# Optimization experiments

Measured on AMD Instinct MI355X. Metric: run time of the kernel, lower is better.

Reference implementation:

```python
import jax, jax.numpy as jnp
import numpy as np

B, T, F, H = 8192, 96, 64, 256


def setup_inputs() -> dict:
    key = jax.random.key(0)
    ks = jax.random.split(key, 8)
    s = 0.05
    return {
        "decoder_feature": jax.random.normal(ks[0], (B, T, F), jnp.float32),
        "init_state": jax.random.normal(ks[1], (B, H), jnp.float32),
        "decoder_init_input": jax.random.normal(ks[2], (B, 1), jnp.float32),
        "kernel": jax.random.normal(ks[3], (1 + F, 3 * H), jnp.float32) * s,
        "recurrent_kernel": jax.random.normal(ks[4], (H, 3 * H), jnp.float32) * s,
        "input_bias": jnp.zeros((3 * H,), jnp.float32),
        "recurrent_bias": jnp.zeros((3 * H,), jnp.float32),
        "dense_w": jax.random.normal(ks[5], (H, 1), jnp.float32) * s,
        "dense_b": jnp.zeros((1,), jnp.float32),
        "predict_seq_length": T,
    }


def reference(decoder_feature, init_state, decoder_init_input, kernel,
              recurrent_kernel, input_bias, recurrent_bias, dense_w, dense_b,
              predict_seq_length):
    # teacher=None, use_attention=False path of Decoder2.forward.
    # Keras GRUCell (reset_after=True) recurrence, scanned over time.
    feats = jnp.swapaxes(decoder_feature[:, :predict_seq_length, :], 0, 1)  # [T,B,F]

    def step(carry, feat_t):
        prev_out, h = carry                                   # [B,1], [B,H]
        x = jnp.concatenate([prev_out, feat_t], axis=-1)      # [B,1+F]
        mx = x @ kernel + input_bias                          # [B,3H]
        mh = h @ recurrent_kernel + recurrent_bias            # [B,3H]
        xz, xr, xh = jnp.split(mx, 3, axis=-1)
        hz, hr, hh = jnp.split(mh, 3, axis=-1)
        z = jax.nn.sigmoid(xz + hz)
        r = jax.nn.sigmoid(xr + hr)
        cand = jnp.tanh(xh + r * hh)
        h_new = z * h + (1.0 - z) * cand
        out = h_new @ dense_w + dense_b                       # [B,1]
        return (out, h_new), out

    _, outs = jax.lax.scan(step, (decoder_init_input, init_state), feats)
    return jnp.swapaxes(outs, 0, 1)                           # [B,T,1]
```

## Files before the change

kernel.cpp:

```cpp
#include <hip/hip_runtime.h>


#define Bdim 8192
#define Tdim 96
#define Fdim 64
#define Hdim 256
#define BM   32
#define XS   72
#define HS   264
#define OS   97

typedef __attribute__((ext_vector_type(8))) short s16x8;
typedef __attribute__((ext_vector_type(4))) float f32x4;

#define MFMA __builtin_amdgcn_mfma_f32_16x16x32_bf16

__device__ __forceinline__ unsigned short f2bf(float f) {
    union { float f; unsigned u; } v; v.f = f;
    unsigned r = v.u + 0x7FFFu + ((v.u >> 16) & 1u);
    return (unsigned short)(r >> 16);
}

__device__ __forceinline__ float sigm_fast(float x) {
    return __builtin_amdgcn_rcpf(1.0f + __expf(-x));
}
__device__ __forceinline__ float tanh_fast(float x) {
    return 1.0f - 2.0f * __builtin_amdgcn_rcpf(1.0f + __expf(2.0f * x));
}

__global__ void prep_swz(const float* __restrict__ Wk, const float* __restrict__ Wr,
                         unsigned short* __restrict__ sW) {
    int idx = blockIdx.x * blockDim.x + threadIdx.x;
    if (idx >= 480 * 64) return;
    int lane = idx & 63, f = idx >> 6;
    int n2 = f & 1;
    int g  = (f >> 1) % 3;
    int kt = (f / 6) % 10;
    int w  = f / 60;
    int q = lane >> 4, cc = lane & 15;
    int n = g * 256 + w * 32 + n2 * 16 + cc;
    unsigned short* d = sW + (size_t)idx * 8;
#pragma unroll
    for (int j = 0; j < 8; ++j) {
        float v;
        if (kt < 8) v = Wr[(size_t)(kt * 32 + q * 8 + j) * 768 + n];
        else        v = Wk[(size_t)(1 + (kt - 8) * 32 + q * 8 + j) * 768 + n];
        d[j] = f2bf(v);
    }
}

__launch_bounds__(1024)
__global__ void gru_mfma9(
    const float* __restrict__ feat,
    const float* __restrict__ init_state,
    const float* __restrict__ init_inp,
    const unsigned short* __restrict__ sW,
    const float* __restrict__ Wk,
    const float* __restrict__ ib, const float* __restrict__ rb,
    const float* __restrict__ dw, const float* __restrict__ db,
    float* __restrict__ out)
{
    __shared__ __align__(16) unsigned short xs[2][BM * XS];
    __shared__ __align__(16) unsigned short hs[2][BM * HS];
    __shared__ float wpart[2][16][BM];
    __shared__ float outbuf[BM * OS];

    const int tid  = threadIdx.x;
    const int lane = tid & 63;
    const int wv   = tid >> 6;
    const int q    = lane >> 4;
    const int c    = lane & 15;
    const int b0   = blockIdx.x * BM;
    const int col  = wv * 16 + c;

    const float bz   = ib[col]       + rb[col];
    const float brr  = ib[256 + col] + rb[256 + col];
    const float bxh  = ib[512 + col];
    const float bhh  = rb[512 + col];
    const float wk0z = Wk[col];
    const float wk0r = Wk[256 + col];
    const float wk0h = Wk[512 + col];
    const float dwv  = dw[col];
    const float dbv  = db[0];

    float hreg[2][4];
    float prevreg[2][4];
#pragma unroll
    for (int mt = 0; mt < 2; ++mt)
#pragma unroll
        for (int i = 0; i < 4; ++i) {
            int row = mt * 16 + q * 4 + i;
            prevreg[mt][i] = init_inp[b0 + row];
            float v = init_state[(size_t)(b0 + row) * Hdim + col];
            hreg[mt][i] = v;
            hs[0][row * HS + col] = f2bf(v);
        }

    {
        int r = tid >> 5, fi = tid & 31;
        float2 f = *(const float2*)&feat[((size_t)(b0 + r) * Tdim + 0) * Fdim + fi * 2];
        ushort2 p; p.x = f2bf(f.x); p.y = f2bf(f.y);
        *(ushort2*)&xs[0][r * XS + fi * 2] = p;
    }

    const unsigned short* wp0 =
        sW + ((size_t)(wv >> 1) * 60 + (wv & 1)) * 512 + lane * 8;

    s16x8 bf[2][3];
#pragma unroll
    for (int g = 0; g < 3; ++g)
        bf[0][g] = *(const s16x8*)(wp0 + (size_t)g * 1024);

    __syncthreads();

    for (int t = 0; t < Tdim; ++t) {
        const unsigned short* hsp = hs[t & 1];
        const unsigned short* xsp = xs[t & 1];

        f32x4 az[2], ar[2], ax[2], ah[2];
#pragma unroll
        for (int mt = 0; mt < 2; ++mt) {
            az[mt] = (f32x4)0.0f; ar[mt] = (f32x4)0.0f;
            ax[mt] = (f32x4)0.0f; ah[mt] = (f32x4)0.0f;
        }

#pragma unroll
        for (int kt = 0; kt < 10; ++kt) {
            if (kt + 1 < 10) {
#pragma unroll
                for (int g = 0; g < 3; ++g)
                    bf[(kt + 1) & 1][g] =
                        *(const s16x8*)(wp0 + (size_t)((kt + 1) * 3 + g) * 1024);
            }
            const s16x8* b = bf[kt & 1];
            s16x8 a0, a1;
            if (kt < 8) {
                a0 = *(const s16x8*)&hsp[c * HS + kt * 32 + q * 8];
                a1 = *(const s16x8*)&hsp[(16 + c) * HS + kt * 32 + q * 8];
            } else {
                a0 = *(const s16x8*)&xsp[c * XS + (kt - 8) * 32 + q * 8];
                a1 = *(const s16x8*)&xsp[(16 + c) * XS + (kt - 8) * 32 + q * 8];
            }
            az[0] = MFMA(a0, b[0], az[0], 0, 0, 0);
            az[1] = MFMA(a1, b[0], az[1], 0, 0, 0);
            ar[0] = MFMA(a0, b[1], ar[0], 0, 0, 0);
            ar[1] = MFMA(a1, b[1], ar[1], 0, 0, 0);
            if (kt < 8) {
                ah[0] = MFMA(a0, b[2], ah[0], 0, 0, 0);
                ah[1] = MFMA(a1, b[2], ah[1], 0, 0, 0);
            } else {
                ax[0] = MFMA(a0, b[2], ax[0], 0, 0, 0);
                ax[1] = MFMA(a1, b[2], ax[1], 0, 0, 0);
            }
        }

#pragma unroll
        for (int g = 0; g < 3; ++g)
            bf[0][g] = *(const s16x8*)(wp0 + (size_t)g * 1024);

        float2 fnext;
        int fr = tid >> 5, ffi = tid & 31;
        if (t + 1 < Tdim)
            fnext = *(const float2*)&feat[((size_t)(b0 + fr) * Tdim + (t + 1)) * Fdim + ffi * 2];

        if (t > 0) {
            int r = lane & 31;
            float s = dbv;
            const float (*wp)[BM] = wpart[(t - 1) & 1];
#pragma unroll
            for (int ww = 0; ww < 16; ++ww) s += wp[ww][r];
            if (wv == 0 && lane < 32) outbuf[r * OS + (t - 1)] = s;
#pragma unroll
            for (int mt = 0; mt < 2; ++mt)
#pragma unroll
                for (int i = 0; i < 4; ++i)
                    prevreg[mt][i] = __shfl(s, mt * 16 + q * 4 + i, 64);
        }

        unsigned short* hsn = hs[(t + 1) & 1];
#pragma unroll
        for (int mt = 0; mt < 2; ++mt)
#pragma unroll
            for (int i = 0; i < 4; ++i) {
                float pv = prevreg[mt][i];
                float zz = sigm_fast(az[mt][i] + bz + pv * wk0z);
                float rr = sigm_fast(ar[mt][i] + brr + pv * wk0r);
                float cd = tanh_fast(ax[mt][i] + bxh + pv * wk0h +
                                     rr * (ah[mt][i] + bhh));
                float hn = zz * hreg[mt][i] + (1.0f - zz) * cd;
                hreg[mt][i] = hn;
                hsn[(mt * 16 + q * 4 + i) * HS + col] = f2bf(hn);
                float s = hn * dwv;
                s += __shfl_xor(s, 1, 64);
                s += __shfl_xor(s, 2, 64);
                s += __shfl_xor(s, 4, 64);
                s += __shfl_xor(s, 8, 64);
                if (c == 0) wpart[t & 1][wv][mt * 16 + q * 4 + i] = s;
            }

        if (t + 1 < Tdim) {
            ushort2 p; p.x = f2bf(fnext.x); p.y = f2bf(fnext.y);
            *(ushort2*)&xs[(t + 1) & 1][fr * XS + ffi * 2] = p;
        }
        __syncthreads();
    }

    {
        int r = lane & 31;
        float s = dbv;
        const float (*wp)[BM] = wpart[(Tdim - 1) & 1];
#pragma unroll
        for (int ww = 0; ww < 16; ++ww) s += wp[ww][r];
        if (wv == 0 && lane < 32) outbuf[r * OS + (Tdim - 1)] = s;
    }
    __syncthreads();

    for (int i = tid; i < BM * Tdim; i += 1024) {
        int r = i / Tdim, tt = i - r * Tdim;
        out[(size_t)b0 * Tdim + i] = outbuf[r * OS + tt];
    }
}

extern "C" void kernel_launch(void* const* d_in, const int* in_sizes, int n_in,
                              void* d_out, int out_size, void* d_ws, size_t ws_size,
                              hipStream_t stream) {
    const float* feat       = (const float*)d_in[0];
    const float* init_state = (const float*)d_in[1];
    const float* init_inp   = (const float*)d_in[2];
    const float* Wk         = (const float*)d_in[3];
    const float* Wr         = (const float*)d_in[4];
    const float* ib         = (const float*)d_in[5];
    const float* rb         = (const float*)d_in[6];
    const float* dw         = (const float*)d_in[7];
    const float* db         = (const float*)d_in[8];
    float* out              = (float*)d_out;

    unsigned short* sW = (unsigned short*)d_ws;

    prep_swz<<<120, 256, 0, stream>>>(Wk, Wr, sW);
    gru_mfma9<<<Bdim / BM, 1024, 0, stream>>>(
        feat, init_state, init_inp, sW, Wk, ib, rb, dw, db, out);
}
```

Measured before the change: 1.644 ms.

## Drop weight register double-buffering and add mid-step barrier for output reduction

Removes the register double-buffered weight fragment prefetch and instead loads the three weight fragments directly in each k-step, which frees registers. Adds a second __syncthreads per timestep, placed after the MFMA phase, so the dense-output partial sums from the previous step are read in the same step rather than deferred. The initial input is seeded into the partial-sum buffer with the bias subtracted, so no special case is needed at t=0. The cost is one extra barrier per timestep and exposed global-load latency for the weights, in exchange for lower register pressure.

```diff
diff --git a/kernel.cpp b/kernel.cpp
--- a/kernel.cpp
+++ b/kernel.cpp
@@ -50,7 +50,7 @@
 }
 
 __launch_bounds__(1024)
-__global__ void gru_mfma9(
+__global__ void gru_mfma11(
     const float* __restrict__ feat,
     const float* __restrict__ init_state,
     const float* __restrict__ init_inp,
@@ -84,17 +84,20 @@
     const float dbv  = db[0];
 
     float hreg[2][4];
-    float prevreg[2][4];
 #pragma unroll
     for (int mt = 0; mt < 2; ++mt)
 #pragma unroll
         for (int i = 0; i < 4; ++i) {
             int row = mt * 16 + q * 4 + i;
-            prevreg[mt][i] = init_inp[b0 + row];
             float v = init_state[(size_t)(b0 + row) * Hdim + col];
             hreg[mt][i] = v;
             hs[0][row * HS + col] = f2bf(v);
         }
+
+    if (tid < 16 * BM) {
+        int ww = tid >> 5, r = tid & 31;
+        wpart[1][ww][r] = (ww == 0) ? (init_inp[b0 + r] - dbv) : 0.0f;
+    }
 
     {
         int r = tid >> 5, fi = tid & 31;
@@ -106,11 +109,6 @@
     const unsigned short* wp0 =
         sW + ((size_t)(wv >> 1) * 60 + (wv & 1)) * 512 + lane * 8;
 
-    s16x8 bf[2][3];
-#pragma unroll
-    for (int g = 0; g < 3; ++g)
-        bf[0][g] = *(const s16x8*)(wp0 + (size_t)g * 1024);
-
     __syncthreads();
 
     for (int t = 0; t < Tdim; ++t) {
@@ -126,13 +124,9 @@
 
 #pragma unroll
         for (int kt = 0; kt < 10; ++kt) {
-            if (kt + 1 < 10) {
-#pragma unroll
-                for (int g = 0; g < 3; ++g)
-                    bf[(kt + 1) & 1][g] =
-                        *(const s16x8*)(wp0 + (size_t)((kt + 1) * 3 + g) * 1024);
-            }
-            const s16x8* b = bf[kt & 1];
+            s16x8 b0f = *(const s16x8*)(wp0 + (size_t)(kt * 3 + 0) * 1024);
+            s16x8 b1f = *(const s16x8*)(wp0 + (size_t)(kt * 3 + 1) * 1024);
+            s16x8 b2f = *(const s16x8*)(wp0 + (size_t)(kt * 3 + 2) * 1024);
             s16x8 a0, a1;
             if (kt < 8) {
                 a0 = *(const s16x8*)&hsp[c * HS + kt * 32 + q * 8];
@@ -141,40 +135,34 @@
                 a0 = *(const s16x8*)&xsp[c * XS + (kt - 8) * 32 + q * 8];
                 a1 = *(const s16x8*)&xsp[(16 + c) * XS + (kt - 8) * 32 + q * 8];
             }
-            az[0] = MFMA(a0, b[0], az[0], 0, 0, 0);
-            az[1] = MFMA(a1, b[0], az[1], 0, 0, 0);
-            ar[0] = MFMA(a0, b[1], ar[0], 0, 0, 0);
-            ar[1] = MFMA(a1, b[1], ar[1], 0, 0, 0);
+            az[0] = MFMA(a0, b0f, az[0], 0, 0, 0);
+            az[1] = MFMA(a1, b0f, az[1], 0, 0, 0);
+            ar[0] = MFMA(a0, b1f, ar[0], 0, 0, 0);
+            ar[1] = MFMA(a1, b1f, ar[1], 0, 0, 0);
             if (kt < 8) {
-                ah[0] = MFMA(a0, b[2], ah[0], 0, 0, 0);
-                ah[1] = MFMA(a1, b[2], ah[1], 0, 0, 0);
+                ah[0] = MFMA(a0, b2f, ah[0], 0, 0, 0);
+                ah[1] = MFMA(a1, b2f, ah[1], 0, 0, 0);
             } else {
-                ax[0] = MFMA(a0, b[2], ax[0], 0, 0, 0);
-                ax[1] = MFMA(a1, b[2], ax[1], 0, 0, 0);
+                ax[0] = MFMA(a0, b2f, ax[0], 0, 0, 0);
+                ax[1] = MFMA(a1, b2f, ax[1], 0, 0, 0);
             }
         }
-
-#pragma unroll
-        for (int g = 0; g < 3; ++g)
-            bf[0][g] = *(const s16x8*)(wp0 + (size_t)g * 1024);
 
         float2 fnext;
         int fr = tid >> 5, ffi = tid & 31;
         if (t + 1 < Tdim)
             fnext = *(const float2*)&feat[((size_t)(b0 + fr) * Tdim + (t + 1)) * Fdim + ffi * 2];
 
-        if (t > 0) {
+        __syncthreads();
+
+        float s;
+        {
             int r = lane & 31;
-            float s = dbv;
+            s = dbv;
             const float (*wp)[BM] = wpart[(t - 1) & 1];
 #pragma unroll
             for (int ww = 0; ww < 16; ++ww) s += wp[ww][r];
-            if (wv == 0 && lane < 32) outbuf[r * OS + (t - 1)] = s;
-#pragma unroll
-            for (int mt = 0; mt < 2; ++mt)
-#pragma unroll
-                for (int i = 0; i < 4; ++i)
-                    prevreg[mt][i] = __shfl(s, mt * 16 + q * 4 + i, 64);
+            if (t > 0 && wv == 0 && lane < 32) outbuf[r * OS + (t - 1)] = s;
         }
 
         unsigned short* hsn = hs[(t + 1) & 1];
@@ -182,7 +170,7 @@
         for (int mt = 0; mt < 2; ++mt)
 #pragma unroll
             for (int i = 0; i < 4; ++i) {
-                float pv = prevreg[mt][i];
+                float pv = __shfl(s, mt * 16 + q * 4 + i, 64);
                 float zz = sigm_fast(az[mt][i] + bz + pv * wk0z);
                 float rr = sigm_fast(ar[mt][i] + brr + pv * wk0r);
                 float cd = tanh_fast(ax[mt][i] + bxh + pv * wk0h +
@@ -190,12 +178,12 @@
                 float hn = zz * hreg[mt][i] + (1.0f - zz) * cd;
                 hreg[mt][i] = hn;
                 hsn[(mt * 16 + q * 4 + i) * HS + col] = f2bf(hn);
-                float s = hn * dwv;
-                s += __shfl_xor(s, 1, 64);
-                s += __shfl_xor(s, 2, 64);
-                s += __shfl_xor(s, 4, 64);
-                s += __shfl_xor(s, 8, 64);
-                if (c == 0) wpart[t & 1][wv][mt * 16 + q * 4 + i] = s;
+                float sp = hn * dwv;
+                sp += __shfl_xor(sp, 1, 64);
+                sp += __shfl_xor(sp, 2, 64);
+                sp += __shfl_xor(sp, 4, 64);
+                sp += __shfl_xor(sp, 8, 64);
+                if (c == 0) wpart[t & 1][wv][mt * 16 + q * 4 + i] = sp;
             }
 
         if (t + 1 < Tdim) {
@@ -238,6 +226,6 @@
     unsigned short* sW = (unsigned short*)d_ws;
 
     prep_swz<<<120, 256, 0, stream>>>(Wk, Wr, sW);
-    gru_mfma9<<<Bdim / BM, 1024, 0, stream>>>(
+    gru_mfma11<<<Bdim / BM, 1024, 0, stream>>>(
         feat, init_state, init_inp, sW, Wk, ib, rb, dw, db, out);
 }
```

Result: slower. 1.831 ms (+11.4%).
